# Kernel optimization log

Measured on AMD Instinct MI355X. Metric: run time of the kernel, lower is better.

## Reference

```python
import jax, jax.numpy as jnp
import numpy as np

ALPHA = 2.0   # spikingjelly surrogate.ATan default
TAU = 2.0     # LIFNode default
VTH = 1.0     # v_threshold
T = 16

@jax.custom_vjp
def atan_spike(u):
    # heaviside forward, ATan surrogate backward
    return (u >= 0).astype(u.dtype)

def _atan_fwd(u):
    return atan_spike(u), u

def _atan_bwd(u, g):
    return (g * (ALPHA / 2.0) / (1.0 + (jnp.pi / 2.0 * ALPHA * u) ** 2),)

atan_spike.defvjp(_atan_fwd, _atan_bwd)


def setup_inputs() -> dict:
    key = jax.random.key(0)
    ks = jax.random.split(key, 7)
    n_in, n_hid, n_out, B = 512, 1024, 6, 16384

    def lin(k, fan_in, shape):
        bound = 1.0 / np.sqrt(fan_in)
        return jax.random.uniform(k, shape, jnp.float32, -bound, bound)

    return {
        "x": jax.random.normal(ks[0], (B, n_in), jnp.float32),
        "W1": lin(ks[1], n_in, (n_hid, n_in)),
        "b1": lin(ks[2], n_in, (n_hid,)),
        "W2": lin(ks[3], n_hid, (n_hid, n_hid)),
        "b2": lin(ks[4], n_hid, (n_hid,)),
        "W3": lin(ks[5], n_hid, (n_out, n_hid)),
        "b3": lin(ks[6], n_hid, (n_out,)),
    }


def reference(x, W1, b1, W2, b2, W3, b3):
    # Input is static across timesteps -> fc1 output is loop-invariant.
    i1 = x @ W1.T + b1  # [B, n_hid]
    B = x.shape[0]
    init = (
        jnp.zeros((B, W1.shape[0]), x.dtype),  # v1
        jnp.zeros((B, W2.shape[0]), x.dtype),  # v2
        jnp.zeros((B, W3.shape[0]), x.dtype),  # v3
    )

    def lif(v, i):
        # charge: v += (i - (v - v_reset)) / tau, v_reset = 0
        v = v + (i - v) / TAU
        s = atan_spike(v - VTH)
        # hard reset to v_reset = 0 (detach_reset=False -> keep grad path)
        v = v * (1.0 - s)
        return v, s

    def step(carry, _):
        v1, v2, v3 = carry
        v1, s1 = lif(v1, i1)
        v2, s2 = lif(v2, s1 @ W2.T + b2)
        v3, s3 = lif(v3, s2 @ W3.T + b3)
        return (v1, v2, v3), s3

    _, spikes = jax.lax.scan(step, init, None, length=T)  # [T, B, n_out]
    return spikes.sum(axis=0) / T
```

## Files before the change

### kernel.cpp

```cpp
#include <hip/hip_runtime.h>
#include <hip/hip_bf16.h>


typedef _Float16 f16;
typedef __attribute__((ext_vector_type(4))) _Float16 f16x4;
typedef __attribute__((ext_vector_type(8))) _Float16 f16x8;
typedef __attribute__((ext_vector_type(4))) float f32x4;

__global__ __launch_bounds__(256) void k_cvt(const float* __restrict__ x,
                                             const float* __restrict__ W1,
                                             f16* __restrict__ xh,
                                             f16* __restrict__ W1h) {
    const int NX = 16384 * 512 / 4;
    const int NW = 1024 * 512 / 4;
    int i = blockIdx.x * 256 + threadIdx.x;
    const int stride = gridDim.x * 256;
    for (; i < NX + NW; i += stride) {
        const float4* src;
        f16* dst;
        int j;
        if (i < NX) { src = (const float4*)x; dst = xh; j = i; }
        else        { src = (const float4*)W1; dst = W1h; j = i - NX; }
        float4 v = src[j];
        f16x4 h;
        h.x = (f16)v.x; h.y = (f16)v.y; h.z = (f16)v.z; h.w = (f16)v.w;
        *(f16x4*)(dst + (size_t)4 * j) = h;
    }
}

__global__ void k_tq(const float* __restrict__ W2, unsigned char* __restrict__ W2u) {
    __shared__ float t[32][33];
    const int bj = blockIdx.x;
    const int bk = blockIdx.y;
    const int tx = threadIdx.x;
    const int ty = threadIdx.y;
#pragma unroll
    for (int i = 0; i < 32; i += 8)
        t[ty + i][tx] = W2[(size_t)(bj * 32 + ty + i) * 1024 + bk * 32 + tx];
    __syncthreads();
#pragma unroll
    for (int i = 0; i < 32; i += 8) {
        float v = t[tx][ty + i];
        int q = (int)rintf(v * 4064.0f);
        q = q > 127 ? 127 : (q < -127 ? -127 : q);
        W2u[(size_t)(bk * 32 + ty + i) * 1024 + bj * 32 + tx] = (unsigned char)(q + 128);
    }
}

__global__ __launch_bounds__(256) void k_fc1(const f16* __restrict__ xh,
                                             const f16* __restrict__ W1h,
                                             const float* __restrict__ b1,
                                             f16* __restrict__ i1h) {
    __shared__ __align__(16) f16 Atile[128 * 32];
    __shared__ __align__(16) f16 Btile[256 * 32];
    const int tid = threadIdx.x;
    const int lane = tid & 63;
    const int wid = tid >> 6;
    const int wm = wid >> 1;
    const int wn = wid & 1;
    const int m0 = blockIdx.x * 128;
    const int n0 = blockIdx.y * 256;

    f32x4 acc[4][8] = {};

    for (int k0 = 0; k0 < 512; k0 += 32) {
        __syncthreads();
#pragma unroll
        for (int q = 0; q < 6; ++q) {
            const bool isA = (q < 2);
            int u = q * 256 + tid;
            int cu = isA ? u : (u - 512);
            int rl = cu >> 2;
            int slot = (cu & 3) ^ (rl & 3);
            const f16* g = isA
                ? xh  + (size_t)(m0 + rl) * 512 + k0 + slot * 8
                : W1h + (size_t)(n0 + rl) * 512 + k0 + slot * 8;
            f16x8 v = *(const f16x8*)g;
            f16* d = (isA ? Atile : Btile) + (size_t)cu * 8;
            *(f16x8*)d = v;
        }
        __syncthreads();
        f16x8 af[4], bf[8];
#pragma unroll
        for (int i = 0; i < 4; ++i) {
            int rowA = (wm << 6) + (i << 4) + (lane & 15);
            af[i] = *(const f16x8*)(Atile + rowA * 32 + (((lane >> 4) ^ (rowA & 3)) << 3));
        }
#pragma unroll
        for (int j = 0; j < 8; ++j) {
            int rowB = (wn << 7) + (j << 4) + (lane & 15);
            bf[j] = *(const f16x8*)(Btile + rowB * 32 + (((lane >> 4) ^ (rowB & 3)) << 3));
        }
#pragma unroll
        for (int i = 0; i < 4; ++i)
#pragma unroll
            for (int j = 0; j < 8; ++j)
                acc[i][j] = __builtin_amdgcn_mfma_f32_16x16x32_f16(af[i], bf[j], acc[i][j], 0, 0, 0);
    }

    float b1v[8];
#pragma unroll
    for (int j = 0; j < 8; ++j)
        b1v[j] = b1[n0 + (wn << 7) + (j << 4) + (lane & 15)];
#pragma unroll
    for (int i = 0; i < 4; ++i) {
        int rm = m0 + (wm << 6) + (i << 4) + ((lane >> 4) << 2);
#pragma unroll
        for (int j = 0; j < 8; ++j) {
            int cn = n0 + (wn << 7) + (j << 4) + (lane & 15);
            f16* op = i1h + (size_t)rm * 1024 + cn;
#pragma unroll
            for (int rr = 0; rr < 4; ++rr)
                op[(size_t)rr * 1024] = (f16)(acc[i][j][rr] + b1v[j]);
        }
    }
}

__global__ __launch_bounds__(256) void k_snn(const f16* __restrict__ i1g,
                                             const unsigned char* __restrict__ W2u,
                                             const float* __restrict__ b2,
                                             const float* __restrict__ W3,
                                             const float* __restrict__ b3,
                                             float* __restrict__ out) {
    const int lane = threadIdx.x & 63;
    const int wid = threadIdx.x >> 6;
    const int r = blockIdx.x * 4 + wid;
    const float DEQ = 1.0f / 4064.0f;

    unsigned train[16];
    unsigned cnt[8] = {};
    const f16x4* i1p4 = (const f16x4*)(i1g + (size_t)r * 1024);
#pragma unroll
    for (int g = 0; g < 4; ++g) {
        f16x4 tq = i1p4[lane + 64 * g];
#pragma unroll
        for (int e = 0; e < 4; ++e) {
            float iv = (float)tq[e];
            float v = 0.0f;
            unsigned tr = 0u;
#pragma unroll
            for (int t = 0; t < 16; ++t) {
                v = v + (iv - v) * 0.5f;
                unsigned su = (v >= 1.0f) ? 1u : 0u;
                v = su ? 0.0f : v;
                tr |= su << t;
                cnt[t >> 1] += su << ((t & 1) * 16);
            }
            train[4 * g + e] = tr;
        }
    }
#pragma unroll
    for (int st = 1; st < 64; st <<= 1)
#pragma unroll
        for (int h = 0; h < 8; ++h)
            cnt[h] += __shfl_xor(cnt[h], st, 64);

    float b2r[16];
#pragma unroll
    for (int q = 0; q < 4; ++q) {
        float4 u = ((const float4*)b2)[lane * 4 + q];
        b2r[4 * q + 0] = u.x; b2r[4 * q + 1] = u.y;
        b2r[4 * q + 2] = u.z; b2r[4 * q + 3] = u.w;
    }
    float b3r[6];
#pragma unroll
    for (int m6 = 0; m6 < 6; ++m6) b3r[m6] = b3[m6];

    const uint4* w2v = (const uint4*)W2u;

    float v2[16] = {}, v3[6] = {}, cnt3[6] = {};

#pragma unroll
    for (int half = 0; half < 2; ++half) {
        unsigned accE[8][4] = {};
        unsigned accO[8][4] = {};
#pragma unroll
        for (int g = 0; g < 4; ++g)
#pragma unroll
            for (int e = 0; e < 4; ++e) {
                unsigned sub = (train[4 * g + e] >> (half * 8)) & 0xFFu;
                unsigned long long m = __ballot(sub != 0u);
                if (m) {
                    int b0 = __builtin_ctzll(m); m &= m - 1;
                    unsigned tr0 = __builtin_amdgcn_readlane(sub, b0);
                    uint4 w0 = w2v[(size_t)(4 * b0 + 256 * g + e) * 64 + lane];
                    while (m) {
                        int b1 = __builtin_ctzll(m); m &= m - 1;
                        unsigned tr1 = __builtin_amdgcn_readlane(sub, b1);
                        uint4 w1 = w2v[(size_t)(4 * b1 + 256 * g + e) * 64 + lane];
                        {
                            unsigned E[4], O[4];
                            E[0] = __builtin_amdgcn_perm(0u, w0.x, 0x04020400u);
                            O[0] = __builtin_amdgcn_perm(0u, w0.x, 0x04030401u);
                            E[1] = __builtin_amdgcn_perm(0u, w0.y, 0x04020400u);
                            O[1] = __builtin_amdgcn_perm(0u, w0.y, 0x04030401u);
                            E[2] = __builtin_amdgcn_perm(0u, w0.z, 0x04020400u);
                            O[2] = __builtin_amdgcn_perm(0u, w0.z, 0x04030401u);
                            E[3] = __builtin_amdgcn_perm(0u, w0.w, 0x04020400u);
                            O[3] = __builtin_amdgcn_perm(0u, w0.w, 0x04030401u);
#pragma unroll
                            for (int tt = 0; tt < 8; ++tt)
                                if (tr0 & (1u << tt)) {
#pragma unroll
                                    for (int d = 0; d < 4; ++d) {
                                        accE[tt][d] += E[d];
                                        accO[tt][d] += O[d];
                                    }
                                }
                        }
                        tr0 = tr1; w0 = w1;
                    }
                    {
                        unsigned E[4], O[4];
                        E[0] = __builtin_amdgcn_perm(0u, w0.x, 0x04020400u);
                        O[0] = __builtin_amdgcn_perm(0u, w0.x, 0x04030401u);
                        E[1] = __builtin_amdgcn_perm(0u, w0.y, 0x04020400u);
                        O[1] = __builtin_amdgcn_perm(0u, w0.y, 0x04030401u);
                        E[2] = __builtin_amdgcn_perm(0u, w0.z, 0x04020400u);
                        O[2] = __builtin_amdgcn_perm(0u, w0.z, 0x04030401u);
                        E[3] = __builtin_amdgcn_perm(0u, w0.w, 0x04020400u);
                        O[3] = __builtin_amdgcn_perm(0u, w0.w, 0x04030401u);
#pragma unroll
                        for (int tt = 0; tt < 8; ++tt)
                            if (tr0 & (1u << tt)) {
#pragma unroll
                                for (int d = 0; d < 4; ++d) {
                                    accE[tt][d] += E[d];
                                    accO[tt][d] += O[d];
                                }
                            }
                    }
                }
            }
#pragma unroll
        for (int tt = 0; tt < 8; ++tt) {
            const int t = half * 8 + tt;
            const int nr = (int)((cnt[t >> 1] >> ((t & 1) * 16)) & 0xFFFFu);
            const int bias = nr << 7;
            bool s2[16];
#pragma unroll
            for (int d = 0; d < 4; ++d) {
                int sq[4];
                sq[0] = (int)(accE[tt][d] & 0xFFFFu) - bias;
                sq[1] = (int)(accO[tt][d] & 0xFFFFu) - bias;
                sq[2] = (int)(accE[tt][d] >> 16) - bias;
                sq[3] = (int)(accO[tt][d] >> 16) - bias;
#pragma unroll
                for (int c = 0; c < 4; ++c) {
                    int e = 4 * d + c;
                    float i2 = fmaf((float)sq[c], DEQ, b2r[e]);
                    float v = v2[e];
                    v = v + (i2 - v) * 0.5f;
                    bool s = v >= 1.0f;
                    s2[e] = s;
                    v2[e] = s ? 0.0f : v;
                }
            }
            float i3[6];
#pragma unroll
            for (int m6 = 0; m6 < 6; ++m6) i3[m6] = b3r[m6];
#pragma unroll
            for (int e = 0; e < 16; ++e) {
                unsigned long long mm = __ballot(s2[e] ? 1 : 0);
                while (mm) {
                    int b = __builtin_ctzll(mm);
                    mm &= mm - 1;
                    int j = 16 * b + e;
#pragma unroll
                    for (int m6 = 0; m6 < 6; ++m6) i3[m6] += W3[m6 * 1024 + j];
                }
            }
#pragma unroll
            for (int m6 = 0; m6 < 6; ++m6) {
                float v = v3[m6];
                v = v + (i3[m6] - v) * 0.5f;
                bool s = v >= 1.0f;
                cnt3[m6] += s ? 1.0f : 0.0f;
                v3[m6] = s ? 0.0f : v;
            }
        }
    }
    if (lane == 0) {
#pragma unroll
        for (int m6 = 0; m6 < 6; ++m6)
            out[(size_t)r * 6 + m6] = cnt3[m6] * 0.0625f;
    }
}

extern "C" void kernel_launch(void* const* d_in, const int* in_sizes, int n_in,
                              void* d_out, int out_size, void* d_ws, size_t ws_size,
                              hipStream_t stream) {
    const float* x  = (const float*)d_in[0];
    const float* W1 = (const float*)d_in[1];
    const float* b1 = (const float*)d_in[2];
    const float* W2 = (const float*)d_in[3];
    const float* b2 = (const float*)d_in[4];
    const float* W3 = (const float*)d_in[5];
    const float* b3 = (const float*)d_in[6];
    float* out = (float*)d_out;

    char* ws = (char*)d_ws;
    f16* i1h = (f16*)ws;
    f16* xh  = (f16*)(ws + ((size_t)32 << 20));
    f16* W1h = (f16*)(ws + ((size_t)48 << 20));
    unsigned char* W2u = (unsigned char*)(ws + ((size_t)49 << 20));

    k_cvt<<<2048, 256, 0, stream>>>(x, W1, xh, W1h);
    k_tq<<<dim3(32, 32), dim3(32, 8), 0, stream>>>(W2, W2u);
    k_fc1<<<dim3(128, 4), 256, 0, stream>>>(xh, W1h, b1, i1h);
    k_snn<<<4096, 256, 0, stream>>>(i1h, W2u, b2, W3, b3, out);
}
```

Before: 380.6 us.

## Fuse fp32-to-fp16 conversion into fc1 loads, use one-wave SNN blocks, skip empty fc3

Removes the separate conversion kernel. fc1 now loads fp32 x and W1 directly and converts to fp16 while staging tiles into shared memory, which avoids writing and re-reading the fp16 copies. The SNN kernel launches one 64-thread block per row with launch bounds (64,4), giving finer scheduling granularity. The per-timestep W3 accumulation is also skipped when no lane fired in layer 2. The cost is that fc1 reads twice as many bytes per tile and does the conversion once per output-column block, so x is converted four times.

```diff
diff --git a/kernel.cpp b/kernel.cpp
--- a/kernel.cpp
+++ b/kernel.cpp
@@ -6,27 +6,6 @@
 typedef __attribute__((ext_vector_type(4))) _Float16 f16x4;
 typedef __attribute__((ext_vector_type(8))) _Float16 f16x8;
 typedef __attribute__((ext_vector_type(4))) float f32x4;
-
-__global__ __launch_bounds__(256) void k_cvt(const float* __restrict__ x,
-                                             const float* __restrict__ W1,
-                                             f16* __restrict__ xh,
-                                             f16* __restrict__ W1h) {
-    const int NX = 16384 * 512 / 4;
-    const int NW = 1024 * 512 / 4;
-    int i = blockIdx.x * 256 + threadIdx.x;
-    const int stride = gridDim.x * 256;
-    for (; i < NX + NW; i += stride) {
-        const float4* src;
-        f16* dst;
-        int j;
-        if (i < NX) { src = (const float4*)x; dst = xh; j = i; }
-        else        { src = (const float4*)W1; dst = W1h; j = i - NX; }
-        float4 v = src[j];
-        f16x4 h;
-        h.x = (f16)v.x; h.y = (f16)v.y; h.z = (f16)v.z; h.w = (f16)v.w;
-        *(f16x4*)(dst + (size_t)4 * j) = h;
-    }
-}
 
 __global__ void k_tq(const float* __restrict__ W2, unsigned char* __restrict__ W2u) {
     __shared__ float t[32][33];
@@ -47,8 +26,8 @@
     }
 }
 
-__global__ __launch_bounds__(256) void k_fc1(const f16* __restrict__ xh,
-                                             const f16* __restrict__ W1h,
+__global__ __launch_bounds__(256) void k_fc1(const float* __restrict__ x,
+                                             const float* __restrict__ W1,
                                              const float* __restrict__ b1,
                                              f16* __restrict__ i1h) {
     __shared__ __align__(16) f16 Atile[128 * 32];
@@ -66,18 +45,22 @@
     for (int k0 = 0; k0 < 512; k0 += 32) {
         __syncthreads();
 #pragma unroll
-        for (int q = 0; q < 6; ++q) {
-            const bool isA = (q < 2);
+        for (int q = 0; q < 12; ++q) {
+            const bool isA = (q < 4);
             int u = q * 256 + tid;
-            int cu = isA ? u : (u - 512);
-            int rl = cu >> 2;
-            int slot = (cu & 3) ^ (rl & 3);
-            const f16* g = isA
-                ? xh  + (size_t)(m0 + rl) * 512 + k0 + slot * 8
-                : W1h + (size_t)(n0 + rl) * 512 + k0 + slot * 8;
-            f16x8 v = *(const f16x8*)g;
-            f16* d = (isA ? Atile : Btile) + (size_t)cu * 8;
-            *(f16x8*)d = v;
+            int cu = isA ? u : (u - 1024);
+            int rl = cu >> 3;
+            int d = (cu >> 1) & 3;
+            int h = cu & 1;
+            int scol = ((d ^ (rl & 3)) << 3) + (h << 2);
+            const float* g = isA
+                ? x  + (size_t)(m0 + rl) * 512 + k0 + scol
+                : W1 + (size_t)(n0 + rl) * 512 + k0 + scol;
+            float4 v = *(const float4*)g;
+            f16x4 hv;
+            hv.x = (f16)v.x; hv.y = (f16)v.y; hv.z = (f16)v.z; hv.w = (f16)v.w;
+            f16* dst = (isA ? Atile : Btile) + (size_t)cu * 4;
+            *(f16x4*)dst = hv;
         }
         __syncthreads();
         f16x8 af[4], bf[8];
@@ -116,15 +99,14 @@
     }
 }
 
-__global__ __launch_bounds__(256) void k_snn(const f16* __restrict__ i1g,
-                                             const unsigned char* __restrict__ W2u,
-                                             const float* __restrict__ b2,
-                                             const float* __restrict__ W3,
-                                             const float* __restrict__ b3,
-                                             float* __restrict__ out) {
+__global__ __launch_bounds__(64, 4) void k_snn(const f16* __restrict__ i1g,
+                                               const unsigned char* __restrict__ W2u,
+                                               const float* __restrict__ b2,
+                                               const float* __restrict__ W3,
+                                               const float* __restrict__ b3,
+                                               float* __restrict__ out) {
     const int lane = threadIdx.x & 63;
-    const int wid = threadIdx.x >> 6;
-    const int r = blockIdx.x * 4 + wid;
+    const int r = blockIdx.x;
     const float DEQ = 1.0f / 4064.0f;
 
     unsigned train[16];
@@ -188,26 +170,24 @@
                         int b1 = __builtin_ctzll(m); m &= m - 1;
                         unsigned tr1 = __builtin_amdgcn_readlane(sub, b1);
                         uint4 w1 = w2v[(size_t)(4 * b1 + 256 * g + e) * 64 + lane];
-                        {
-                            unsigned E[4], O[4];
-                            E[0] = __builtin_amdgcn_perm(0u, w0.x, 0x04020400u);
-                            O[0] = __builtin_amdgcn_perm(0u, w0.x, 0x04030401u);
-                            E[1] = __builtin_amdgcn_perm(0u, w0.y, 0x04020400u);
-                            O[1] = __builtin_amdgcn_perm(0u, w0.y, 0x04030401u);
-                            E[2] = __builtin_amdgcn_perm(0u, w0.z, 0x04020400u);
-                            O[2] = __builtin_amdgcn_perm(0u, w0.z, 0x04030401u);
-                            E[3] = __builtin_amdgcn_perm(0u, w0.w, 0x04020400u);
-                            O[3] = __builtin_amdgcn_perm(0u, w0.w, 0x04030401u);
-#pragma unroll
-                            for (int tt = 0; tt < 8; ++tt)
-                                if (tr0 & (1u << tt)) {
-#pragma unroll
-                                    for (int d = 0; d < 4; ++d) {
-                                        accE[tt][d] += E[d];
-                                        accO[tt][d] += O[d];
-                                    }
+                        unsigned E[4], O[4];
+                        E[0] = __builtin_amdgcn_perm(0u, w0.x, 0x04020400u);
+                        O[0] = __builtin_amdgcn_perm(0u, w0.x, 0x04030401u);
+                        E[1] = __builtin_amdgcn_perm(0u, w0.y, 0x04020400u);
+                        O[1] = __builtin_amdgcn_perm(0u, w0.y, 0x04030401u);
+                        E[2] = __builtin_amdgcn_perm(0u, w0.z, 0x04020400u);
+                        O[2] = __builtin_amdgcn_perm(0u, w0.z, 0x04030401u);
+                        E[3] = __builtin_amdgcn_perm(0u, w0.w, 0x04020400u);
+                        O[3] = __builtin_amdgcn_perm(0u, w0.w, 0x04030401u);
+#pragma unroll
+                        for (int tt = 0; tt < 8; ++tt)
+                            if (tr0 & (1u << tt)) {
+#pragma unroll
+                                for (int d = 0; d < 4; ++d) {
+                                    accE[tt][d] += E[d];
+                                    accO[tt][d] += O[d];
                                 }
-                        }
+                            }
                         tr0 = tr1; w0 = w1;
                     }
                     {
@@ -238,6 +218,7 @@
             const int nr = (int)((cnt[t >> 1] >> ((t & 1) * 16)) & 0xFFFFu);
             const int bias = nr << 7;
             bool s2[16];
+            bool any2 = false;
 #pragma unroll
             for (int d = 0; d < 4; ++d) {
                 int sq[4];
@@ -253,21 +234,24 @@
                     v = v + (i2 - v) * 0.5f;
                     bool s = v >= 1.0f;
                     s2[e] = s;
+                    any2 |= s;
                     v2[e] = s ? 0.0f : v;
                 }
             }
             float i3[6];
 #pragma unroll
             for (int m6 = 0; m6 < 6; ++m6) i3[m6] = b3r[m6];
-#pragma unroll
-            for (int e = 0; e < 16; ++e) {
-                unsigned long long mm = __ballot(s2[e] ? 1 : 0);
-                while (mm) {
-                    int b = __builtin_ctzll(mm);
-                    mm &= mm - 1;
-                    int j = 16 * b + e;
-#pragma unroll
-                    for (int m6 = 0; m6 < 6; ++m6) i3[m6] += W3[m6 * 1024 + j];
+            if (__ballot(any2 ? 1 : 0)) {
+#pragma unroll
+                for (int e = 0; e < 16; ++e) {
+                    unsigned long long mm = __ballot(s2[e] ? 1 : 0);
+                    while (mm) {
+                        int b = __builtin_ctzll(mm);
+                        mm &= mm - 1;
+                        int j = 16 * b + e;
+#pragma unroll
+                        for (int m6 = 0; m6 < 6; ++m6) i3[m6] += W3[m6 * 1024 + j];
+                    }
                 }
             }
 #pragma unroll
@@ -301,12 +285,9 @@
 
     char* ws = (char*)d_ws;
     f16* i1h = (f16*)ws;
-    f16* xh  = (f16*)(ws + ((size_t)32 << 20));
-    f16* W1h = (f16*)(ws + ((size_t)48 << 20));
-    unsigned char* W2u = (unsigned char*)(ws + ((size_t)49 << 20));
-
-    k_cvt<<<2048, 256, 0, stream>>>(x, W1, xh, W1h);
+    unsigned char* W2u = (unsigned char*)(ws + ((size_t)32 << 20));
+
     k_tq<<<dim3(32, 32), dim3(32, 8), 0, stream>>>(W2, W2u);
-    k_fc1<<<dim3(128, 4), 256, 0, stream>>>(xh, W1h, b1, i1h);
-    k_snn<<<4096, 256, 0, stream>>>(i1h, W2u, b2, W3, b3, out);
-}
+    k_fc1<<<dim3(128, 4), 256, 0, stream>>>(x, W1, b1, i1h);
+    k_snn<<<16384, 64, 0, stream>>>(i1h, W2u, b2, W3, b3, out);
+}
```

After: 369.3 us. 1.03x faster.
